# Kernel tuning notes

Hardware: AMD Instinct MI355X
Metric: run time of the kernel (lower is better)

Reference implementation:

```python
import jax, jax.numpy as jnp
import numpy as np
from jax import lax

N_NODES = 150_000
N_EDGES = 1_500_000
N_GRAPHS = 150          # batch_size(30) * sequence_length(5), hardcoded in forward
BATCH_SIZE = 30
SEQ_LEN = 5
IN_F = 1
HID = 100               # gcn_hidden_size == lstm_hidden_size


def setup_inputs() -> dict:
    key = jax.random.key(0)
    ks = jax.random.split(key, 12)
    x = jax.random.normal(ks[0], (N_NODES, IN_F), dtype=jnp.float32)
    edge_index = jax.random.randint(ks[1], (2, N_EDGES), 0, N_NODES, dtype=jnp.int32)
    # 150 graphs of 1000 nodes each (contiguous, as PyG batching produces)
    batch = jnp.repeat(jnp.arange(N_GRAPHS, dtype=jnp.int32), N_NODES // N_GRAPHS)
    s = 0.1
    params = {
        # GCNConv layer 1: Linear(no bias) weight stored [in, out]; separate bias
        "W1": jax.random.normal(ks[2], (IN_F, HID), jnp.float32) * s,
        "b1": jnp.zeros((HID,), jnp.float32),
        # GCNConv layer 2
        "W2": jax.random.normal(ks[3], (HID, HID), jnp.float32) * s,
        "b2": jnp.zeros((HID,), jnp.float32),
        # LSTM (PyTorch gate order i,f,g,o), weights [4H, in]/[4H, H]
        "W_ih": jax.random.normal(ks[4], (4 * HID, HID), jnp.float32) * s,
        "W_hh": jax.random.normal(ks[5], (4 * HID, HID), jnp.float32) * s,
        "b_ih": jnp.zeros((4 * HID,), jnp.float32),
        "b_hh": jnp.zeros((4 * HID,), jnp.float32),
        # output head Linear(HID, 1)
        "W_out": jax.random.normal(ks[6], (1, HID), jnp.float32) * s,
        "b_out": jnp.zeros((1,), jnp.float32),
    }
    return {"x": x, "edge_index": edge_index, "batch": batch, **params}


def _gcn_conv(x, src, dst, W, b, n_nodes):
    """PyG GCNConv: h = W x; out = D^-1/2 (A+I) D^-1/2 h + b."""
    h = x @ W  # [N, HID]
    deg = jax.ops.segment_sum(jnp.ones_like(dst, dtype=h.dtype), dst, num_segments=n_nodes)
    dinv = lax.rsqrt(deg)  # deg >= 1 thanks to self loops
    norm = dinv[src] * dinv[dst]  # [E+N]
    msg = h[src] * norm[:, None]  # gather + scale (memory-bound hot loop)
    out = jax.ops.segment_sum(msg, dst, num_segments=n_nodes)
    return out + b


def _lstm_last_hidden(xs, W_ih, W_hh, b_ih, b_hh):
    """xs: [B, T, H] -> last hidden state [B, H] (single-layer LSTM)."""
    B = xs.shape[0]
    H = W_hh.shape[1]
    h0 = jnp.zeros((B, H), xs.dtype)
    c0 = jnp.zeros((B, H), xs.dtype)

    def step(carry, xt):
        h, c = carry
        gates = xt @ W_ih.T + h @ W_hh.T + (b_ih + b_hh)
        i, f, g, o = jnp.split(gates, 4, axis=-1)
        c = jax.nn.sigmoid(f) * c + jax.nn.sigmoid(i) * jnp.tanh(g)
        h = jax.nn.sigmoid(o) * jnp.tanh(c)
        return (h, c), None

    (h_last, _), _ = lax.scan(step, (h0, c0), jnp.swapaxes(xs, 0, 1))
    return h_last


def reference(x, edge_index, batch, W1, b1, W2, b2, W_ih, W_hh, b_ih, b_hh, W_out, b_out):
    n_nodes = x.shape[0]
    loops = jnp.arange(n_nodes, dtype=edge_index.dtype)
    src = jnp.concatenate([edge_index[0], loops])
    dst = jnp.concatenate([edge_index[1], loops])

    h = _gcn_conv(x, src, dst, W1, b1, n_nodes)
    h = _gcn_conv(h, src, dst, W2, b2, n_nodes)

    # global mean pool over 150 graphs
    sums = jax.ops.segment_sum(h, batch, num_segments=N_GRAPHS)
    cnts = jax.ops.segment_sum(jnp.ones((n_nodes,), h.dtype), batch, num_segments=N_GRAPHS)
    pooled = sums / jnp.maximum(cnts, 1.0)[:, None]  # [150, HID]

    seq = pooled.reshape(BATCH_SIZE, SEQ_LEN, -1)  # [30, 5, HID]
    h_last = _lstm_last_hidden(seq, W_ih, W_hh, b_ih, b_hh)
    prediction = h_last @ W_out.T + b_out  # [30, 1]
    return prediction
```

## Files before the change

kernel.cpp:

```cpp
#include <hip/hip_runtime.h>
#include <math.h>

#define N_NODES   150000
#define N_EDGES   1500000
#define N_GRAPHS  150
#define HID       100
#define BATCH     30
#define SEQ       5
#define NODES_PER_GRAPH 1000

#define NPB   256
#define NB    586
#define SBLK  512
#define EPB   2932
#define CAP   3584

__global__ __launch_bounds__(256) void k_sort(const int* __restrict__ src,
                                              const int* __restrict__ dst,
                                              int* __restrict__ bucketCount,
                                              unsigned int* __restrict__ sorted) {
    __shared__ unsigned int   epack[EPB];
    __shared__ unsigned short ebuck[EPB];
    __shared__ int hist[NB];
    __shared__ int baseS[NB];
    int t = threadIdx.x;
    for (int i = t; i < NB; i += 256) hist[i] = 0;
    __syncthreads();
    int base = blockIdx.x * EPB;
    int end  = min(base + EPB, N_EDGES);
    for (int i = base + t * 4; i < end; i += 1024) {
        int4 s4 = *reinterpret_cast<const int4*>(src + i);
        int4 d4 = *reinterpret_cast<const int4*>(dst + i);
        int l = i - base;
        int sv[4] = { s4.x, s4.y, s4.z, s4.w };
        int dl[4] = { d4.x & 255, d4.y & 255, d4.z & 255, d4.w & 255 };
        int bk[4] = { d4.x >> 8, d4.y >> 8, d4.z >> 8, d4.w >> 8 };
        #pragma unroll
        for (int k = 0; k < 4; ++k) {
            atomicAdd(&hist[bk[k]], 1);
            epack[l + k] = ((unsigned int)sv[k] << 8) | (unsigned int)dl[k];
            ebuck[l + k] = (unsigned short)bk[k];
        }
    }
    __syncthreads();
    for (int j = t; j < NB; j += 256) {
        int c = hist[j];
        int gb = (c > 0) ? atomicAdd(&bucketCount[j], c) : 0;
        baseS[j] = j * CAP + gb;
    }
    __syncthreads();
    for (int j = t; j < NB; j += 256) hist[j] = 0;
    __syncthreads();
    int nloc = end - base;
    for (int l = t; l < nloc; l += 256) {
        int bk = ebuck[l];
        int idx = atomicAdd(&hist[bk], 1);
        sorted[baseS[bk] + idx] = epack[l];
    }
}

__device__ __forceinline__ void bin2_reduce_store(float val, int thresh,
                                                  float* red, int t,
                                                  float2* __restrict__ outp) {
    red[t] = (t < thresh) ? val : 0.0f;
    __syncthreads();
    for (int s = 128; s > 0; s >>= 1) {
        if (t < s) red[t] += red[t + s];
        __syncthreads();
    }
    float b0 = red[0];
    __syncthreads();
    red[t] = (t >= thresh) ? val : 0.0f;
    __syncthreads();
    for (int s = 128; s > 0; s >>= 1) {
        if (t < s) red[t] += red[t + s];
        __syncthreads();
    }
    if (t == 0) *outp = make_float2(b0, red[0]);
}

__global__ __launch_bounds__(256) void k_accA(const unsigned int* __restrict__ sorted,
                                              const int* __restrict__ bucketCount,
                                              const float* __restrict__ x,
                                              float* __restrict__ pd,
                                              float* __restrict__ px,
                                              float2* __restrict__ pW) {
    __shared__ int degI[2][NPB];
    __shared__ float red[256];
    int b = blockIdx.x;
    int t = threadIdx.x;
    int n0 = b << 8;
    int nn = min(NPB, N_NODES - n0);
    degI[0][t] = 0; degI[1][t] = 0;
    __syncthreads();
    int e0 = b * CAP, e1 = e0 + bucketCount[b];
    int rep = t & 1;
    int nvec = (e1 - e0) >> 2;
    for (int v = t; v < nvec; v += 256) {
        uint4 u4 = *reinterpret_cast<const uint4*>(sorted + e0 + v * 4);
        atomicAdd(&degI[rep][u4.x & 255], 1);
        atomicAdd(&degI[rep][u4.y & 255], 1);
        atomicAdd(&degI[rep][u4.z & 255], 1);
        atomicAdd(&degI[rep][u4.w & 255], 1);
    }
    int tail0 = e0 + (nvec << 2);
    if (tail0 + t < e1) atomicAdd(&degI[rep][sorted[tail0 + t] & 255], 1);
    __syncthreads();
    float val = 0.0f;
    if (t < nn) {
        float dv = 1.0f / sqrtf((float)(1 + degI[0][t] + degI[1][t]));
        pd[n0 + t] = dv;
        px[n0 + t] = dv * x[n0 + t];
        val = dv * dv;
    }
    int g0 = n0 / 1000;
    int thresh = (g0 + 1) * 1000 - n0;
    bin2_reduce_store(val, thresh, red, t, &pW[b]);
}

__global__ __launch_bounds__(256) void k_accB(const unsigned int* __restrict__ sorted,
                                              const int* __restrict__ bucketCount,
                                              const float* __restrict__ pd,
                                              const float* __restrict__ px,
                                              float2* __restrict__ pa2,
                                              float2* __restrict__ pA) {
    __shared__ float t1s[2][NPB];
    __shared__ float red[256];
    int b = blockIdx.x;
    int t = threadIdx.x;
    int n0 = b << 8;
    int nn = min(NPB, N_NODES - n0);
    t1s[0][t] = 0.0f; t1s[1][t] = 0.0f;
    __syncthreads();
    int e0 = b * CAP, e1 = e0 + bucketCount[b];
    int rep = t & 1;
    int nvec = (e1 - e0) >> 2;
    for (int v = t; v < nvec; v += 256) {
        uint4 u4 = *reinterpret_cast<const uint4*>(sorted + e0 + v * 4);
        float p0 = px[u4.x >> 8];
        float p1 = px[u4.y >> 8];
        float p2 = px[u4.z >> 8];
        float p3 = px[u4.w >> 8];
        atomicAdd(&t1s[rep][u4.x & 255], p0);
        atomicAdd(&t1s[rep][u4.y & 255], p1);
        atomicAdd(&t1s[rep][u4.z & 255], p2);
        atomicAdd(&t1s[rep][u4.w & 255], p3);
    }
    int tail0 = e0 + (nvec << 2);
    if (tail0 + t < e1) {
        unsigned int u = sorted[tail0 + t];
        atomicAdd(&t1s[rep][u & 255], px[u >> 8]);
    }
    __syncthreads();
    float val = 0.0f;
    if (t < nn) {
        float dv = pd[n0 + t];
        float T1 = t1s[0][t] + t1s[1][t];
        float agg1 = dv * T1 + dv * px[n0 + t];
        float a1 = dv * agg1;
        pa2[n0 + t] = make_float2(dv, a1);
        val = dv * a1;
    }
    int g0 = n0 / 1000;
    int thresh = (g0 + 1) * 1000 - n0;
    bin2_reduce_store(val, thresh, red, t, &pA[b]);
}

__global__ __launch_bounds__(256) void k_accG(const unsigned int* __restrict__ sorted,
                                              const int* __restrict__ bucketCount,
                                              const float* __restrict__ pd,
                                              const float2* __restrict__ pa2,
                                              float4* __restrict__ pG) {
    __shared__ float dvl[NPB];
    __shared__ float4 red4[256];
    int b = blockIdx.x;
    int t = threadIdx.x;
    int n0 = b << 8;
    int nn = min(NPB, N_NODES - n0);
    dvl[t] = (t < nn) ? pd[n0 + t] : 0.0f;
    __syncthreads();
    int g0 = n0 / 1000;
    int thresh = (g0 + 1) * 1000 - n0;
    float sa0 = 0.f, sa1 = 0.f, sw0 = 0.f, sw1 = 0.f;
    int e0 = b * CAP, e1 = e0 + bucketCount[b];
    auto proc = [&](unsigned int u) {
        int dl = (int)(u & 255);
        float dvd = dvl[dl];
        float2 v = pa2[u >> 8];
        if (dl < thresh) { sw0 += dvd * v.x; sa0 += dvd * v.y; }
        else             { sw1 += dvd * v.x; sa1 += dvd * v.y; }
    };
    int nvec = (e1 - e0) >> 2;
    for (int v = t; v < nvec; v += 256) {
        uint4 u4 = *reinterpret_cast<const uint4*>(sorted + e0 + v * 4);
        proc(u4.x); proc(u4.y); proc(u4.z); proc(u4.w);
    }
    int tail0 = e0 + (nvec << 2);
    if (tail0 + t < e1) proc(sorted[tail0 + t]);
    red4[t] = make_float4(sa0, sa1, sw0, sw1);
    __syncthreads();
    for (int s = 128; s > 0; s >>= 1) {
        if (t < s) {
            red4[t].x += red4[t + s].x; red4[t].y += red4[t + s].y;
            red4[t].z += red4[t + s].z; red4[t].w += red4[t + s].w;
        }
        __syncthreads();
    }
    if (t == 0) pG[b] = red4[0];
}

__global__ __launch_bounds__(512) void k_tail(const float2* __restrict__ pW,
                                              const float2* __restrict__ pA,
                                              const float4* __restrict__ pG,
                                              const float* __restrict__ W1,
                                              const float* __restrict__ b1,
                                              const float* __restrict__ W2,
                                              const float* __restrict__ b2,
                                              const float* __restrict__ W_ih,
                                              const float* __restrict__ W_hh,
                                              const float* __restrict__ b_ih,
                                              const float* __restrict__ b_hh,
                                              const float* __restrict__ W_out,
                                              const float* __restrict__ b_out,
                                              float* __restrict__ outp) {
    int b = blockIdx.x;
    int t = threadIdx.x;
    __shared__ float gA[N_GRAPHS], gW[N_GRAPHS];
    __shared__ float v1[HID], v2[HID];
    __shared__ float xs_l[SEQ][HID];
    __shared__ float Xg_l[SEQ][4 * HID];
    __shared__ float hs[HID], cs[HID], gsb[4 * HID];
    __shared__ float red[512];

    if (t < N_GRAPHS) { gA[t] = 0.0f; gW[t] = 0.0f; }
    __syncthreads();
    for (int j = t; j < NB; j += 512) {
        int n0 = j << 8;
        int g0 = n0 / 1000;
        float2 w2v = pW[j];
        float2 a2v = pA[j];
        float4 g4 = pG[j];
        atomicAdd(&gA[g0], a2v.x + g4.x);
        atomicAdd(&gW[g0], w2v.x + g4.z);
        if (g0 + 1 < N_GRAPHS) {
            atomicAdd(&gA[g0 + 1], a2v.y + g4.y);
            atomicAdd(&gW[g0 + 1], w2v.y + g4.w);
        }
    }
    if (t < HID) {
        float a = 0.0f, c = 0.0f;
        for (int k = 0; k < HID; ++k) {
            float w2 = W2[k * HID + t];
            a += W1[k] * w2;
            c += b1[k] * w2;
        }
        v1[t] = a; v2[t] = c;
    }
    __syncthreads();

    if (t < SEQ * HID) {
        int s = t / HID, j = t - s * HID;
        int g = b * SEQ + s;
        float ma = gA[g] * (1.0f / NODES_PER_GRAPH);
        float mw = gW[g] * (1.0f / NODES_PER_GRAPH);
        xs_l[s][j] = ma * v1[j] + mw * v2[j] + b2[j];
    }
    __syncthreads();

    float wreg[HID];
    if (t < 4 * HID) {
        const float4* wp = reinterpret_cast<const float4*>(W_ih + t * HID);
        #pragma unroll
        for (int q = 0; q < HID / 4; ++q) {
            float4 w4 = wp[q];
            wreg[4*q+0] = w4.x; wreg[4*q+1] = w4.y; wreg[4*q+2] = w4.z; wreg[4*q+3] = w4.w;
        }
        float bias = b_ih[t] + b_hh[t];
        for (int s = 0; s < SEQ; ++s) {
            float acc = bias;
            #pragma unroll
            for (int k = 0; k < HID; ++k)
                acc += xs_l[s][k] * wreg[k];
            Xg_l[s][t] = acc;
        }
        wp = reinterpret_cast<const float4*>(W_hh + t * HID);
        #pragma unroll
        for (int q = 0; q < HID / 4; ++q) {
            float4 w4 = wp[q];
            wreg[4*q+0] = w4.x; wreg[4*q+1] = w4.y; wreg[4*q+2] = w4.z; wreg[4*q+3] = w4.w;
        }
    }
    if (t < HID) { hs[t] = 0.0f; cs[t] = 0.0f; }
    __syncthreads();

    for (int step = 0; step < SEQ; ++step) {
        if (t < 4 * HID) {
            float acc = Xg_l[step][t];
            #pragma unroll
            for (int k = 0; k < HID; ++k)
                acc += hs[k] * wreg[k];
            gsb[t] = acc;
        }
        __syncthreads();
        if (t < HID) {
            float ig = 1.0f / (1.0f + expf(-gsb[t]));
            float fg = 1.0f / (1.0f + expf(-gsb[HID + t]));
            float gg = tanhf(gsb[2 * HID + t]);
            float og = 1.0f / (1.0f + expf(-gsb[3 * HID + t]));
            float c  = fg * cs[t] + ig * gg;
            cs[t] = c;
            hs[t] = og * tanhf(c);
        }
        __syncthreads();
    }

    float v = (t < HID) ? hs[t] * W_out[t] : 0.0f;
    red[t] = v;
    __syncthreads();
    for (int s = 256; s > 0; s >>= 1) {
        if (t < s) red[t] += red[t + s];
        __syncthreads();
    }
    if (t == 0) outp[b] = red[0] + b_out[0];
}

static inline char* align_up(char* p, size_t a) {
    return (char*)(((uintptr_t)p + (a - 1)) & ~(uintptr_t)(a - 1));
}

extern "C" void kernel_launch(void* const* d_in, const int* in_sizes, int n_in,
                              void* d_out, int out_size, void* d_ws, size_t ws_size,
                              hipStream_t stream) {
    const float* x    = (const float*)d_in[0];
    const int*   ei   = (const int*)d_in[1];
    const int*   srcp = ei;
    const int*   dstp = ei + N_EDGES;
    const float* W1   = (const float*)d_in[3];
    const float* b1   = (const float*)d_in[4];
    const float* W2   = (const float*)d_in[5];
    const float* b2   = (const float*)d_in[6];
    const float* W_ih = (const float*)d_in[7];
    const float* W_hh = (const float*)d_in[8];
    const float* b_ih = (const float*)d_in[9];
    const float* b_hh = (const float*)d_in[10];
    const float* W_out= (const float*)d_in[11];
    const float* b_out= (const float*)d_in[12];
    float* out = (float*)d_out;

    char* w = (char*)d_ws;
    int*  bucketCount = (int*)w;             w = align_up(w + NB * sizeof(int), 64);
    unsigned int* sorted = (unsigned int*)w; w = align_up(w + (size_t)NB * CAP * sizeof(unsigned int), 64);
    float*  pd  = (float*)w;                 w = align_up(w + (size_t)N_NODES * sizeof(float), 64);
    float*  px  = (float*)w;                 w = align_up(w + (size_t)N_NODES * sizeof(float), 64);
    float2* pa2 = (float2*)w;                w = align_up(w + (size_t)N_NODES * sizeof(float2), 64);
    float2* pW  = (float2*)w;                w = align_up(w + NB * sizeof(float2), 64);
    float2* pA  = (float2*)w;                w = align_up(w + NB * sizeof(float2), 64);
    float4* pG  = (float4*)w;                w = align_up(w + NB * sizeof(float4), 64);

    hipMemsetAsync(bucketCount, 0, NB * sizeof(int), stream);
    k_sort<<<SBLK, 256, 0, stream>>>(srcp, dstp, bucketCount, sorted);
    k_accA<<<NB, 256, 0, stream>>>(sorted, bucketCount, x, pd, px, pW);
    k_accB<<<NB, 256, 0, stream>>>(sorted, bucketCount, pd, px, pa2, pA);
    k_accG<<<NB, 256, 0, stream>>>(sorted, bucketCount, pd, pa2, pG);
    k_tail<<<BATCH, 512, 0, stream>>>(pW, pA, pG, W1, b1, W2, b2,
                                      W_ih, W_hh, b_ih, b_hh, W_out, b_out, out);
}
```

Measured before the change: 91.76 us.

## Split edge bucketing into histogram, column scan and scatter; widen buckets to 512 nodes

Replaces the single-pass bucket sort, which staged edges in LDS and reserved bucket slots with global atomics, with three kernels. The first builds per-block histograms, the second does a column prefix scan, and the third scatters each edge directly to a deterministic position. Buckets now cover 512 nodes instead of 256, which halves the number of accumulation blocks. Each thread in those blocks now handles two nodes and reduces a float2 pair in one pass rather than two. The cost is extra launches, a second read of dst, and fewer, larger blocks with more edges each for the accumulation kernels.

```diff
diff --git a/kernel.cpp b/kernel.cpp
--- a/kernel.cpp
+++ b/kernel.cpp
@@ -9,74 +9,91 @@
 #define SEQ       5
 #define NODES_PER_GRAPH 1000
 
-#define NPB   256
-#define NB    586
-#define SBLK  512
-#define EPB   2932
-#define CAP   3584
-
-__global__ __launch_bounds__(256) void k_sort(const int* __restrict__ src,
-                                              const int* __restrict__ dst,
-                                              int* __restrict__ bucketCount,
-                                              unsigned int* __restrict__ sorted) {
-    __shared__ unsigned int   epack[EPB];
-    __shared__ unsigned short ebuck[EPB];
+#define NPB   512
+#define NB    293
+#define SBLK  128
+#define SORT_T 512
+#define EPB   11720
+#define CAP   5632
+#define DLMASK 511
+
+__global__ __launch_bounds__(SORT_T) void k_s1(const int* __restrict__ dst,
+                                               int* __restrict__ blockBase) {
     __shared__ int hist[NB];
-    __shared__ int baseS[NB];
-    int t = threadIdx.x;
-    for (int i = t; i < NB; i += 256) hist[i] = 0;
+    int t = threadIdx.x;
+    for (int i = t; i < NB; i += SORT_T) hist[i] = 0;
     __syncthreads();
     int base = blockIdx.x * EPB;
     int end  = min(base + EPB, N_EDGES);
-    for (int i = base + t * 4; i < end; i += 1024) {
+    for (int i = base + t * 4; i < end; i += SORT_T * 4) {
+        int4 d = *reinterpret_cast<const int4*>(dst + i);
+        atomicAdd(&hist[d.x >> 9], 1);
+        atomicAdd(&hist[d.y >> 9], 1);
+        atomicAdd(&hist[d.z >> 9], 1);
+        atomicAdd(&hist[d.w >> 9], 1);
+    }
+    __syncthreads();
+    for (int j = t; j < NB; j += SORT_T)
+        blockBase[blockIdx.x * NB + j] = hist[j];
+}
+
+__global__ __launch_bounds__(SBLK) void k_colscan(int* __restrict__ blockBase,
+                                                  int* __restrict__ bucketCount) {
+    __shared__ int v[SBLK];
+    int j = blockIdx.x;
+    int t = threadIdx.x;
+    int val = blockBase[t * NB + j];
+    v[t] = val;
+    __syncthreads();
+    for (int off = 1; off < SBLK; off <<= 1) {
+        int w = (t >= off) ? v[t - off] : 0;
+        __syncthreads();
+        v[t] += w;
+        __syncthreads();
+    }
+    blockBase[t * NB + j] = v[t] - val;
+    if (t == SBLK - 1) bucketCount[j] = v[t];
+}
+
+__global__ __launch_bounds__(SORT_T) void k_s2(const int* __restrict__ src,
+                                               const int* __restrict__ dst,
+                                               const int* __restrict__ blockBase,
+                                               unsigned int* __restrict__ sorted) {
+    __shared__ int cursor[NB];
+    __shared__ int baseS[NB];
+    int t = threadIdx.x;
+    const int* bb = blockBase + blockIdx.x * NB;
+    for (int i = t; i < NB; i += SORT_T) {
+        cursor[i] = 0;
+        baseS[i] = i * CAP + bb[i];
+    }
+    __syncthreads();
+    int base = blockIdx.x * EPB;
+    int end  = min(base + EPB, N_EDGES);
+    for (int i = base + t * 4; i < end; i += SORT_T * 4) {
         int4 s4 = *reinterpret_cast<const int4*>(src + i);
         int4 d4 = *reinterpret_cast<const int4*>(dst + i);
-        int l = i - base;
+        int bk[4] = { d4.x >> 9, d4.y >> 9, d4.z >> 9, d4.w >> 9 };
         int sv[4] = { s4.x, s4.y, s4.z, s4.w };
-        int dl[4] = { d4.x & 255, d4.y & 255, d4.z & 255, d4.w & 255 };
-        int bk[4] = { d4.x >> 8, d4.y >> 8, d4.z >> 8, d4.w >> 8 };
+        int dl[4] = { d4.x & DLMASK, d4.y & DLMASK, d4.z & DLMASK, d4.w & DLMASK };
         #pragma unroll
         for (int k = 0; k < 4; ++k) {
-            atomicAdd(&hist[bk[k]], 1);
-            epack[l + k] = ((unsigned int)sv[k] << 8) | (unsigned int)dl[k];
-            ebuck[l + k] = (unsigned short)bk[k];
-        }
-    }
-    __syncthreads();
-    for (int j = t; j < NB; j += 256) {
-        int c = hist[j];
-        int gb = (c > 0) ? atomicAdd(&bucketCount[j], c) : 0;
-        baseS[j] = j * CAP + gb;
-    }
-    __syncthreads();
-    for (int j = t; j < NB; j += 256) hist[j] = 0;
-    __syncthreads();
-    int nloc = end - base;
-    for (int l = t; l < nloc; l += 256) {
-        int bk = ebuck[l];
-        int idx = atomicAdd(&hist[bk], 1);
-        sorted[baseS[bk] + idx] = epack[l];
-    }
-}
-
-__device__ __forceinline__ void bin2_reduce_store(float val, int thresh,
-                                                  float* red, int t,
+            int b = bk[k];
+            int idx = atomicAdd(&cursor[b], 1);
+            sorted[baseS[b] + idx] = ((unsigned int)sv[k] << 9) | (unsigned int)dl[k];
+        }
+    }
+}
+
+__device__ __forceinline__ void bin2_reduce_store(float2 acc, float2* red2, int t,
                                                   float2* __restrict__ outp) {
-    red[t] = (t < thresh) ? val : 0.0f;
+    red2[t] = acc;
     __syncthreads();
     for (int s = 128; s > 0; s >>= 1) {
-        if (t < s) red[t] += red[t + s];
-        __syncthreads();
-    }
-    float b0 = red[0];
-    __syncthreads();
-    red[t] = (t >= thresh) ? val : 0.0f;
-    __syncthreads();
-    for (int s = 128; s > 0; s >>= 1) {
-        if (t < s) red[t] += red[t + s];
-        __syncthreads();
-    }
-    if (t == 0) *outp = make_float2(b0, red[0]);
+        if (t < s) { red2[t].x += red2[t + s].x; red2[t].y += red2[t + s].y; }
+        __syncthreads();
+    }
+    if (t == 0) *outp = red2[0];
 }
 
 __global__ __launch_bounds__(256) void k_accA(const unsigned int* __restrict__ sorted,
@@ -86,36 +103,42 @@
                                               float* __restrict__ px,
                                               float2* __restrict__ pW) {
     __shared__ int degI[2][NPB];
-    __shared__ float red[256];
+    __shared__ float2 red2[256];
     int b = blockIdx.x;
     int t = threadIdx.x;
-    int n0 = b << 8;
+    int n0 = b << 9;
     int nn = min(NPB, N_NODES - n0);
-    degI[0][t] = 0; degI[1][t] = 0;
+    degI[0][t] = 0; degI[0][t + 256] = 0;
+    degI[1][t] = 0; degI[1][t + 256] = 0;
     __syncthreads();
     int e0 = b * CAP, e1 = e0 + bucketCount[b];
     int rep = t & 1;
     int nvec = (e1 - e0) >> 2;
     for (int v = t; v < nvec; v += 256) {
         uint4 u4 = *reinterpret_cast<const uint4*>(sorted + e0 + v * 4);
-        atomicAdd(&degI[rep][u4.x & 255], 1);
-        atomicAdd(&degI[rep][u4.y & 255], 1);
-        atomicAdd(&degI[rep][u4.z & 255], 1);
-        atomicAdd(&degI[rep][u4.w & 255], 1);
+        atomicAdd(&degI[rep][u4.x & DLMASK], 1);
+        atomicAdd(&degI[rep][u4.y & DLMASK], 1);
+        atomicAdd(&degI[rep][u4.z & DLMASK], 1);
+        atomicAdd(&degI[rep][u4.w & DLMASK], 1);
     }
     int tail0 = e0 + (nvec << 2);
-    if (tail0 + t < e1) atomicAdd(&degI[rep][sorted[tail0 + t] & 255], 1);
-    __syncthreads();
-    float val = 0.0f;
-    if (t < nn) {
-        float dv = 1.0f / sqrtf((float)(1 + degI[0][t] + degI[1][t]));
-        pd[n0 + t] = dv;
-        px[n0 + t] = dv * x[n0 + t];
-        val = dv * dv;
-    }
+    if (tail0 + t < e1) atomicAdd(&degI[rep][sorted[tail0 + t] & DLMASK], 1);
+    __syncthreads();
     int g0 = n0 / 1000;
     int thresh = (g0 + 1) * 1000 - n0;
-    bin2_reduce_store(val, thresh, red, t, &pW[b]);
+    float2 acc = make_float2(0.f, 0.f);
+    #pragma unroll
+    for (int h = 0; h < 2; ++h) {
+        int slot = t + h * 256;
+        if (slot < nn) {
+            float dv = 1.0f / sqrtf((float)(1 + degI[0][slot] + degI[1][slot]));
+            pd[n0 + slot] = dv;
+            px[n0 + slot] = dv * x[n0 + slot];
+            float v = dv * dv;
+            if (slot < thresh) acc.x += v; else acc.y += v;
+        }
+    }
+    bin2_reduce_store(acc, red2, t, &pW[b]);
 }
 
 __global__ __launch_bounds__(256) void k_accB(const unsigned int* __restrict__ sorted,
@@ -125,45 +148,51 @@
                                               float2* __restrict__ pa2,
                                               float2* __restrict__ pA) {
     __shared__ float t1s[2][NPB];
-    __shared__ float red[256];
+    __shared__ float2 red2[256];
     int b = blockIdx.x;
     int t = threadIdx.x;
-    int n0 = b << 8;
+    int n0 = b << 9;
     int nn = min(NPB, N_NODES - n0);
-    t1s[0][t] = 0.0f; t1s[1][t] = 0.0f;
+    t1s[0][t] = 0.0f; t1s[0][t + 256] = 0.0f;
+    t1s[1][t] = 0.0f; t1s[1][t + 256] = 0.0f;
     __syncthreads();
     int e0 = b * CAP, e1 = e0 + bucketCount[b];
     int rep = t & 1;
     int nvec = (e1 - e0) >> 2;
     for (int v = t; v < nvec; v += 256) {
         uint4 u4 = *reinterpret_cast<const uint4*>(sorted + e0 + v * 4);
-        float p0 = px[u4.x >> 8];
-        float p1 = px[u4.y >> 8];
-        float p2 = px[u4.z >> 8];
-        float p3 = px[u4.w >> 8];
-        atomicAdd(&t1s[rep][u4.x & 255], p0);
-        atomicAdd(&t1s[rep][u4.y & 255], p1);
-        atomicAdd(&t1s[rep][u4.z & 255], p2);
-        atomicAdd(&t1s[rep][u4.w & 255], p3);
+        float p0 = px[u4.x >> 9];
+        float p1 = px[u4.y >> 9];
+        float p2 = px[u4.z >> 9];
+        float p3 = px[u4.w >> 9];
+        atomicAdd(&t1s[rep][u4.x & DLMASK], p0);
+        atomicAdd(&t1s[rep][u4.y & DLMASK], p1);
+        atomicAdd(&t1s[rep][u4.z & DLMASK], p2);
+        atomicAdd(&t1s[rep][u4.w & DLMASK], p3);
     }
     int tail0 = e0 + (nvec << 2);
     if (tail0 + t < e1) {
         unsigned int u = sorted[tail0 + t];
-        atomicAdd(&t1s[rep][u & 255], px[u >> 8]);
-    }
-    __syncthreads();
-    float val = 0.0f;
-    if (t < nn) {
-        float dv = pd[n0 + t];
-        float T1 = t1s[0][t] + t1s[1][t];
-        float agg1 = dv * T1 + dv * px[n0 + t];
-        float a1 = dv * agg1;
-        pa2[n0 + t] = make_float2(dv, a1);
-        val = dv * a1;
-    }
+        atomicAdd(&t1s[rep][u & DLMASK], px[u >> 9]);
+    }
+    __syncthreads();
     int g0 = n0 / 1000;
     int thresh = (g0 + 1) * 1000 - n0;
-    bin2_reduce_store(val, thresh, red, t, &pA[b]);
+    float2 acc = make_float2(0.f, 0.f);
+    #pragma unroll
+    for (int h = 0; h < 2; ++h) {
+        int slot = t + h * 256;
+        if (slot < nn) {
+            float dv = pd[n0 + slot];
+            float T1 = t1s[0][slot] + t1s[1][slot];
+            float agg1 = dv * T1 + dv * px[n0 + slot];
+            float a1 = dv * agg1;
+            pa2[n0 + slot] = make_float2(dv, a1);
+            float v = dv * a1;
+            if (slot < thresh) acc.x += v; else acc.y += v;
+        }
+    }
+    bin2_reduce_store(acc, red2, t, &pA[b]);
 }
 
 __global__ __launch_bounds__(256) void k_accG(const unsigned int* __restrict__ sorted,
@@ -175,18 +204,19 @@
     __shared__ float4 red4[256];
     int b = blockIdx.x;
     int t = threadIdx.x;
-    int n0 = b << 8;
+    int n0 = b << 9;
     int nn = min(NPB, N_NODES - n0);
-    dvl[t] = (t < nn) ? pd[n0 + t] : 0.0f;
+    dvl[t]       = (t < nn)       ? pd[n0 + t]       : 0.0f;
+    dvl[t + 256] = (t + 256 < nn) ? pd[n0 + t + 256] : 0.0f;
     __syncthreads();
     int g0 = n0 / 1000;
     int thresh = (g0 + 1) * 1000 - n0;
     float sa0 = 0.f, sa1 = 0.f, sw0 = 0.f, sw1 = 0.f;
     int e0 = b * CAP, e1 = e0 + bucketCount[b];
     auto proc = [&](unsigned int u) {
-        int dl = (int)(u & 255);
+        int dl = (int)(u & DLMASK);
         float dvd = dvl[dl];
-        float2 v = pa2[u >> 8];
+        float2 v = pa2[u >> 9];
         if (dl < thresh) { sw0 += dvd * v.x; sa0 += dvd * v.y; }
         else             { sw1 += dvd * v.x; sa1 += dvd * v.y; }
     };
@@ -235,7 +265,7 @@
     if (t < N_GRAPHS) { gA[t] = 0.0f; gW[t] = 0.0f; }
     __syncthreads();
     for (int j = t; j < NB; j += 512) {
-        int n0 = j << 8;
+        int n0 = j << 9;
         int g0 = n0 / 1000;
         float2 w2v = pW[j];
         float2 a2v = pA[j];
@@ -349,6 +379,7 @@
 
     char* w = (char*)d_ws;
     int*  bucketCount = (int*)w;             w = align_up(w + NB * sizeof(int), 64);
+    int*  blockBase   = (int*)w;             w = align_up(w + (size_t)SBLK * NB * sizeof(int), 64);
     unsigned int* sorted = (unsigned int*)w; w = align_up(w + (size_t)NB * CAP * sizeof(unsigned int), 64);
     float*  pd  = (float*)w;                 w = align_up(w + (size_t)N_NODES * sizeof(float), 64);
     float*  px  = (float*)w;                 w = align_up(w + (size_t)N_NODES * sizeof(float), 64);
@@ -357,11 +388,12 @@
     float2* pA  = (float2*)w;                w = align_up(w + NB * sizeof(float2), 64);
     float4* pG  = (float4*)w;                w = align_up(w + NB * sizeof(float4), 64);
 
-    hipMemsetAsync(bucketCount, 0, NB * sizeof(int), stream);
-    k_sort<<<SBLK, 256, 0, stream>>>(srcp, dstp, bucketCount, sorted);
-    k_accA<<<NB, 256, 0, stream>>>(sorted, bucketCount, x, pd, px, pW);
-    k_accB<<<NB, 256, 0, stream>>>(sorted, bucketCount, pd, px, pa2, pA);
-    k_accG<<<NB, 256, 0, stream>>>(sorted, bucketCount, pd, pa2, pG);
-    k_tail<<<BATCH, 512, 0, stream>>>(pW, pA, pG, W1, b1, W2, b2,
-                                      W_ih, W_hh, b_ih, b_hh, W_out, b_out, out);
-}
+    k_s1     <<<SBLK, SORT_T, 0, stream>>>(dstp, blockBase);
+    k_colscan<<<NB, SBLK, 0, stream>>>(blockBase, bucketCount);
+    k_s2     <<<SBLK, SORT_T, 0, stream>>>(srcp, dstp, blockBase, sorted);
+    k_accA   <<<NB, 256, 0, stream>>>(sorted, bucketCount, x, pd, px, pW);
+    k_accB   <<<NB, 256, 0, stream>>>(sorted, bucketCount, pd, px, pa2, pA);
+    k_accG   <<<NB, 256, 0, stream>>>(sorted, bucketCount, pd, pa2, pG);
+    k_tail   <<<BATCH, 512, 0, stream>>>(pW, pA, pG, W1, b1, W2, b2,
+                                         W_ih, W_hh, b_ih, b_hh, W_out, b_out, out);
+}
```

New measurement: 82.33 us. 1.11x faster.
